# Optimization experiments

Hardware: AMD Instinct MI355X
Metric: run time of the kernel (lower is better)

Reference implementation:

```python
import jax, jax.numpy as jnp
import numpy as np
from jax import lax

K = 3; PAD = 1; STR = 1; DIL = 1; DG = 16; MRM = 10.0


def _conv3(x, w, b):
    y = lax.conv_general_dilated(x, w, (1, 1), ((PAD, PAD), (PAD, PAD)),
                                 dimension_numbers=('NCHW', 'OIHW', 'NCHW'))
    return y + b[None, :, None, None]


def _leaky(x):
    return jnp.where(x >= 0, x, 0.1 * x)


def _bilinear_gather(img, py, px):
    # img: [B, dg, cg, H, W]; py, px: [B, dg, KK, H, W] sampling coords
    B, dg, cg, H, W = img.shape
    KK = py.shape[2]
    y0f = jnp.floor(py); x0f = jnp.floor(px)
    wy = py - y0f; wx = px - x0f          # bilinear fractions (grad flows via py/px)
    y0 = y0f.astype(jnp.int32); x0 = x0f.astype(jnp.int32)
    y1 = y0 + 1; x1 = x0 + 1
    imgf = img.reshape(B * dg, cg, H * W)

    def gather(yi, xi):
        valid = ((yi >= 0) & (yi < H) & (xi >= 0) & (xi < W)).astype(img.dtype)
        idx = jnp.clip(yi, 0, H - 1) * W + jnp.clip(xi, 0, W - 1)
        idxf = idx.reshape(B * dg, KK * H * W)
        v = jax.vmap(lambda im, ix: im[:, ix])(imgf, idxf)  # [B*dg, cg, KK*H*W]
        v = v.reshape(B, dg, cg, KK, H, W)
        return v * valid[:, :, None]  # zero padding outside image

    w00 = ((1 - wy) * (1 - wx))[:, :, None]
    w01 = ((1 - wy) * wx)[:, :, None]
    w10 = (wy * (1 - wx))[:, :, None]
    w11 = (wy * wx)[:, :, None]
    return (gather(y0, x0) * w00 + gather(y0, x1) * w01 +
            gather(y1, x0) * w10 + gather(y1, x1) * w11)


def reference(x, extra_feat, flow, w1, b1, w2, b2, w3, b3, weight):
    B, C, H, W = x.shape
    KK = K * K
    cg = C // DG
    P = DG * KK
    # offset/mask generating convnet
    h = _leaky(_conv3(extra_feat, w1, b1))
    h = _leaky(_conv3(h, w2, b2))
    o = _conv3(h, w3, b3)                       # [B, 3*P, H, W]
    o1, o2, m = jnp.split(o, 3, axis=1)
    off = MRM * jnp.tanh(jnp.concatenate([o1, o2], axis=1))  # [B, 2P, H, W]
    flow_yx = flow[:, ::-1]                      # flip(1): (x,y)->(y,x)
    off = off + jnp.tile(flow_yx, (1, P, 1, 1))
    off = off.reshape(B, DG, KK, 2, H, W)        # pair p=(g,k): channel 2p=y, 2p+1=x
    off_y = off[:, :, :, 0]
    off_x = off[:, :, :, 1]
    mask = jax.nn.sigmoid(m).reshape(B, DG, KK, H, W)

    ki = jnp.arange(KK)
    ky = (ki // K).astype(x.dtype) * DIL - PAD   # kernel row offsets
    kx = (ki % K).astype(x.dtype) * DIL - PAD
    base_h = jnp.arange(H, dtype=x.dtype) * STR
    base_w = jnp.arange(W, dtype=x.dtype) * STR
    py = base_h[None, None, None, :, None] + ky[None, None, :, None, None] + off_y
    px = base_w[None, None, None, None, :] + kx[None, None, :, None, None] + off_x

    img = x.reshape(B, DG, cg, H, W)
    val = _bilinear_gather(img, py, px) * mask[:, :, None]  # [B,dg,cg,KK,H,W]
    wk = weight.reshape(weight.shape[0], DG, cg, KK)
    # modulated deformable conv accumulate (bias=None in original forward)
    return jnp.einsum('bgckhw,ogck->bohw', val, wk)


def setup_inputs() -> dict:
    key = jax.random.key(0)
    ks = jax.random.split(key, 10)
    B, C, H, W = 2, 64, 128, 128
    OFFC = 3 * K * K * DG  # 432
    return {
        'x': jax.random.normal(ks[0], (B, C, H, W), jnp.float32),
        'extra_feat': jax.random.normal(ks[1], (B, 2 * C, H, W), jnp.float32),
        'flow': jax.random.normal(ks[2], (B, 2, H, W), jnp.float32),
        'w1': jax.random.normal(ks[3], (C, 2 * C, 3, 3), jnp.float32) * 0.05,
        'b1': jnp.zeros((C,), jnp.float32),
        'w2': jax.random.normal(ks[4], (C, C, 3, 3), jnp.float32) * 0.05,
        'b2': jnp.zeros((C,), jnp.float32),
        'w3': jax.random.normal(ks[5], (OFFC, C, 3, 3), jnp.float32) * 0.01,
        'b3': jnp.zeros((OFFC,), jnp.float32),
        'weight': jax.random.normal(ks[6], (C, C, 3, 3), jnp.float32) * 0.05,
    }
```

## Files before the change

### kernel.cpp

```cpp
#include <hip/hip_runtime.h>
#include <math.h>

constexpr int B_   = 2;
constexpr int C_   = 64;
constexpr int H_   = 128;
constexpr int W_   = 128;
constexpr int HW_  = H_ * W_;
constexpr int DG_  = 16;
constexpr int KK_  = 9;
constexpr int CG_  = 4;
constexpr int OFFC_ = 3 * KK_ * DG_;
constexpr int R_   = C_ * KK_;
constexpr int WP_  = 130;
constexpr int HWP_ = WP_ * WP_;

typedef _Float16 half8 __attribute__((ext_vector_type(8)));
typedef _Float16 half4 __attribute__((ext_vector_type(4)));
typedef float floatx4 __attribute__((ext_vector_type(4)));

__device__ __forceinline__ void gl_lds16(const _Float16* g, _Float16* l)
{
    __builtin_amdgcn_global_load_lds(
        (const __attribute__((address_space(1))) void*)g,
        (__attribute__((address_space(3))) void*)l, 16, 0, 0);
}

__device__ __forceinline__ int afrag_src(int c)
{
    const int cmf = c >> 6, cq = (c >> 4) & 3, cl = c & 15;
    return (cmf * 16 + cl) * 32 + cq * 8;
}

template <int OC, int CIN>
__global__ __launch_bounds__(256) void prep_wA_k(
    const float* __restrict__ w, _Float16* __restrict__ wA)
{
    constexpr int CH = CIN / 32;
    const int j = blockIdx.x * 256 + threadIdx.x;
    if (j >= 9 * CH * OC * 32) return;
    const int slab = j / (OC * 32);
    const int rem  = j - slab * (OC * 32);
    const int oc   = rem >> 5;
    const int jj   = rem & 31;
    const int t    = slab / CH;
    const int h    = slab - t * CH;
    const int ic   = h * 32 + jj;
    wA[j] = (_Float16)w[(size_t)oc * (CIN * 9) + ic * 9 + t];
}

__global__ __launch_bounds__(256) void prep_wkA_k(
    const float* __restrict__ wk, _Float16* __restrict__ wkA)
{
    const int j = blockIdx.x * 256 + threadIdx.x;
    if (j >= 18 * 64 * 32) return;
    const int s   = j >> 11;
    const int rem = j & 2047;
    const int oc  = rem >> 5;
    const int jj  = rem & 31;
    const int k   = s >> 1;
    const int gc  = (s & 1) * 32 + jj;
    wkA[j] = (_Float16)wk[(size_t)oc * R_ + gc * 9 + k];
}

template <int CC>
__global__ __launch_bounds__(256) void nchw2slabpad_f16_k(
    const float* __restrict__ in, _Float16* __restrict__ outh)
{
    const int pix = blockIdx.x * 256 + threadIdx.x;
    const int b   = blockIdx.y;
    const int yp  = pix >> 7;
    const int xp  = pix & (W_ - 1);
    const float* ib = in + (size_t)b * CC * HW_ + pix;
#pragma unroll
    for (int c0 = 0; c0 < CC; c0 += 8) {
        half8 v;
#pragma unroll
        for (int j = 0; j < 8; ++j)
            v[j] = (_Float16)ib[(size_t)(c0 + j) * HW_];
        const int slab = c0 >> 5;
        *(half8*)&outh[((size_t)(slab * B_ + b) * HWP_
                        + (size_t)(yp + 1) * WP_ + (xp + 1)) * 32 + (c0 & 31)] = v;
    }
}

__global__ __launch_bounds__(256) void nchw2gx_f16_k(
    const float* __restrict__ in, _Float16* __restrict__ outh)
{
    const int pix = blockIdx.x * 256 + threadIdx.x;
    const int b   = blockIdx.y;
    const float* ib = in + (size_t)b * C_ * HW_ + pix;
#pragma unroll
    for (int g = 0; g < DG_; ++g) {
        half4 v;
#pragma unroll
        for (int c = 0; c < 4; ++c)
            v[c] = (_Float16)ib[(size_t)(g * 4 + c) * HW_];
        *(half4*)&outh[((size_t)(b * DG_ + g) * HW_ + pix) * 4] = v;
    }
}

__global__ __launch_bounds__(256, 2) void conv1_mfma_k(
    const _Float16* __restrict__ inp, const _Float16* __restrict__ wA,
    const float* __restrict__ bias, _Float16* __restrict__ outp)
{
    __shared__ __align__(16) _Float16 Asm[2 * 4096];

    const int tid  = threadIdx.x;
    const int lane = tid & 63;
    const int wv   = tid >> 6;
    const int l15  = lane & 15;
    const int quad = lane >> 4;

    const int zx   = blockIdx.x;
    const int row  = zx >> 1;
    const int b    = row >> 7;
    const int y    = row & 127;
    const int px0  = (zx & 1) * 64 + wv * 16;

    const int sA = afrag_src(tid);

    floatx4 acc[4];
#pragma unroll
    for (int mf = 0; mf < 4; ++mf)
        acc[mf] = (floatx4){0.f, 0.f, 0.f, 0.f};

    half8 Bf[2][2];

    gl_lds16(wA + 0 * 2048 + sA, Asm + 0 * 2048 + tid * 8);
    gl_lds16(wA + 1 * 2048 + sA, Asm + 1 * 2048 + tid * 8);
#pragma unroll
    for (int j = 0; j < 2; ++j)
        Bf[0][j] = *(const half8*)&inp[
            ((size_t)(j * B_ + b) * HWP_ + (size_t)(y + 0) * WP_
             + (px0 + l15 + 0)) * 32 + quad * 8];
    __syncthreads();

#pragma unroll
    for (int p = 0; p < 18; ++p) {
        const int cur = p & 1, nxt = cur ^ 1;
        if (p < 17) {
            const int ks0 = 2 * p + 2;
            const int t = ks0 >> 2;
            const int h0 = ks0 & 3;
            const int dy = t / 3, dx = t % 3;
#pragma unroll
            for (int j = 0; j < 2; ++j) {
                gl_lds16(wA + (size_t)(ks0 + j) * 2048 + sA,
                         Asm + (nxt * 2 + j) * 2048 + tid * 8);
                Bf[nxt][j] = *(const half8*)&inp[
                    ((size_t)((h0 + j) * B_ + b) * HWP_ + (size_t)(y + dy) * WP_
                     + (px0 + l15 + dx)) * 32 + quad * 8];
            }
        }
#pragma unroll
        for (int j = 0; j < 2; ++j) {
            const _Float16* abase = Asm + (cur * 2 + j) * 2048 + lane * 8;
#pragma unroll
            for (int mf = 0; mf < 4; ++mf) {
                const half8 afr = *(const half8*)&abase[mf * 512];
                acc[mf] = __builtin_amdgcn_mfma_f32_16x16x32_f16(afr, Bf[cur][j], acc[mf], 0, 0, 0);
            }
        }
        __syncthreads();
    }

#pragma unroll
    for (int mf = 0; mf < 4; ++mf) {
        const int oc4 = mf * 16 + quad * 4;
        const float4 b4 = *(const float4*)&bias[oc4];
        half4 v4;
#pragma unroll
        for (int reg = 0; reg < 4; ++reg) {
            float r = acc[mf][reg] + ((const float*)&b4)[reg];
            r = (r >= 0.f) ? r : 0.1f * r;
            v4[reg] = (_Float16)r;
        }
        *(half4*)&outp[((size_t)((oc4 >> 5) * B_ + b) * HWP_
                        + (size_t)(y + 1) * WP_ + (px0 + l15 + 1)) * 32 + (oc4 & 31)] = v4;
    }
}

__global__ __launch_bounds__(256, 2) void conv2_mfma_k(
    const _Float16* __restrict__ inp, const _Float16* __restrict__ wA,
    const float* __restrict__ bias, _Float16* __restrict__ outp)
{
    __shared__ __align__(16) _Float16 Asm[18 * 2048];

    const int tid  = threadIdx.x;
    const int lane = tid & 63;
    const int wv   = tid >> 6;
    const int l15  = lane & 15;
    const int quad = lane >> 4;

    const int zx   = blockIdx.x;
    const int row  = zx >> 1;
    const int b    = row >> 7;
    const int y    = row & 127;
    const int px0  = (zx & 1) * 64 + wv * 16;

    const int sA = afrag_src(tid);

#pragma unroll
    for (int s = 0; s < 18; ++s)
        gl_lds16(wA + (size_t)s * 2048 + sA, Asm + s * 2048 + tid * 8);

    const _Float16* bb[6];
#pragma unroll
    for (int h = 0; h < 2; ++h)
#pragma unroll
        for (int dy = 0; dy < 3; ++dy)
            bb[h * 3 + dy] = inp + ((size_t)(h * B_ + b) * HWP_
                                    + (size_t)(y + dy) * WP_ + px0 + l15) * 32 + quad * 8;

    floatx4 acc[4];
#pragma unroll
    for (int mf = 0; mf < 4; ++mf)
        acc[mf] = (floatx4){0.f, 0.f, 0.f, 0.f};

    __syncthreads();

    const _Float16* abase = Asm + lane * 8;
#pragma unroll
    for (int ks = 0; ks < 18; ++ks) {
        const int t = ks >> 1, h = ks & 1;
        const int dy = t / 3, dx = t % 3;
        const half8 bfr = *(const half8*)&bb[h * 3 + dy][dx * 32];
#pragma unroll
        for (int mf = 0; mf < 4; ++mf) {
            const half8 afr = *(const half8*)&abase[ks * 2048 + mf * 512];
            acc[mf] = __builtin_amdgcn_mfma_f32_16x16x32_f16(afr, bfr, acc[mf], 0, 0, 0);
        }
    }

#pragma unroll
    for (int mf = 0; mf < 4; ++mf) {
        const int oc4 = mf * 16 + quad * 4;
        const float4 b4 = *(const float4*)&bias[oc4];
        half4 v4;
#pragma unroll
        for (int reg = 0; reg < 4; ++reg) {
            float r = acc[mf][reg] + ((const float*)&b4)[reg];
            r = (r >= 0.f) ? r : 0.1f * r;
            v4[reg] = (_Float16)r;
        }
        *(half4*)&outp[((size_t)((oc4 >> 5) * B_ + b) * HWP_
                        + (size_t)(y + 1) * WP_ + (px0 + l15 + 1)) * 32 + (oc4 & 31)] = v4;
    }
}

__global__ __launch_bounds__(256, 3) void conv3_mfma_k(
    const _Float16* __restrict__ h2p, const _Float16* __restrict__ w3A,
    const float* __restrict__ bias, const float* __restrict__ flow,
    _Float16* __restrict__ omh)
{
    __shared__ __align__(16) _Float16 Smem[17 * 1536];
    _Float16* Lds = Smem;

    const int tid  = threadIdx.x;
    const int lane = tid & 63;
    const int wv   = tid >> 6;
    const int l15  = lane & 15;
    const int quad = lane >> 4;

    const int row = blockIdx.x;
    const int b   = row >> 7;
    const int y   = row & 127;
    const int m0  = blockIdx.y * 48;
    const int px0 = wv * 32;

#pragma unroll
    for (int r = 0; r < 13; ++r) {
        const int c = r * 256 + tid;
        if (c < 17 * 192) {
            const int ks = c / 192;
            const int cl = c - ks * 192;
            const int cmf = cl >> 6, cq = (cl >> 4) & 3, ccl = cl & 15;
            gl_lds16(w3A + ((size_t)ks * OFFC_ + m0 + cmf * 16 + ccl) * 32 + cq * 8,
                     Smem + c * 8);
        }
    }

    half8 Af17[3];
#pragma unroll
    for (int mf = 0; mf < 3; ++mf)
        Af17[mf] = *(const half8*)&w3A[
            ((size_t)17 * OFFC_ + m0 + mf * 16 + l15) * 32 + quad * 8];

    const _Float16* bb[6];
#pragma unroll
    for (int h = 0; h < 2; ++h)
#pragma unroll
        for (int dy = 0; dy < 3; ++dy)
            bb[h * 3 + dy] = h2p + ((size_t)(h * B_ + b) * HWP_
                                    + (size_t)(y + dy) * WP_ + px0 + l15) * 32 + quad * 8;

    floatx4 acc[3][2];
#pragma unroll
    for (int mf = 0; mf < 3; ++mf)
#pragma unroll
        for (int nf = 0; nf < 2; ++nf)
            acc[mf][nf] = (floatx4){0.f, 0.f, 0.f, 0.f};

    __syncthreads();

    const _Float16* abase = Smem + lane * 8;
#pragma unroll
    for (int ks = 0; ks < 17; ++ks) {
        const int t = ks >> 1, h = ks & 1;
        const int dy = t / 3, dx = t % 3;
        const half8 b0 = *(const half8*)&bb[h * 3 + dy][dx * 32];
        const half8 b1 = *(const half8*)&bb[h * 3 + dy][(16 + dx) * 32];
#pragma unroll
        for (int mf = 0; mf < 3; ++mf) {
            const half8 afr = *(const half8*)&abase[ks * 1536 + mf * 512];
            acc[mf][0] = __builtin_amdgcn_mfma_f32_16x16x32_f16(afr, b0, acc[mf][0], 0, 0, 0);
            acc[mf][1] = __builtin_amdgcn_mfma_f32_16x16x32_f16(afr, b1, acc[mf][1], 0, 0, 0);
        }
    }
    {
        const half8 b0 = *(const half8*)&bb[5][2 * 32];
        const half8 b1 = *(const half8*)&bb[5][(16 + 2) * 32];
#pragma unroll
        for (int mf = 0; mf < 3; ++mf) {
            acc[mf][0] = __builtin_amdgcn_mfma_f32_16x16x32_f16(Af17[mf], b0, acc[mf][0], 0, 0, 0);
            acc[mf][1] = __builtin_amdgcn_mfma_f32_16x16x32_f16(Af17[mf], b1, acc[mf][1], 0, 0, 0);
        }
    }
    __syncthreads();

    const bool is_off = (blockIdx.y < 6);
    float flY[2], flX[2];
#pragma unroll
    for (int nf = 0; nf < 2; ++nf) {
        const int px = px0 + nf * 16 + l15;
        if (is_off) {
            flY[nf] = flow[(size_t)(b * 2 + 1) * HW_ + y * W_ + px];
            flX[nf] = flow[(size_t)(b * 2 + 0) * HW_ + y * W_ + px];
        }
    }
#pragma unroll
    for (int mf = 0; mf < 3; ++mf) {
        const float4 b4 = *(const float4*)&bias[m0 + mf * 16 + quad * 4];
#pragma unroll
        for (int nf = 0; nf < 2; ++nf) {
            const int px = px0 + nf * 16 + l15;
#pragma unroll
            for (int reg = 0; reg < 4; ++reg) {
                const int ocl = mf * 16 + quad * 4 + reg;
                float val = acc[mf][nf][reg] + ((const float*)&b4)[reg];
                if (is_off) {
                    const int slot = reg & 1;
                    const float fl = slot ? flX[nf] : flY[nf];
                    const float e = __expf(2.f * val);
                    val = 10.f * (1.f - __fdividef(2.f, e + 1.f)) + fl;
                } else {
                    val = __fdividef(1.f, 1.f + __expf(-val));
                }
                Lds[ocl * 132 + px] = (_Float16)val;
            }
        }
    }
    __syncthreads();

#pragma unroll
    for (int it = 0; it < 6; ++it) {
        const int j4 = it * 256 + tid;
        const int r  = j4 >> 5;
        const int c4 = j4 & 31;
        const int oc = m0 + r;
        int g, k, slot;
        if (oc < 2 * DG_ * KK_) {
            g = oc / 18;
            const int rem = oc - g * 18;
            k = rem >> 1;
            slot = rem & 1;
        } else {
            const int c = oc - 2 * DG_ * KK_;
            g = c / 9;
            k = c - g * 9;
            slot = 2;
        }
        const half4 hv = *(const half4*)&Lds[r * 132 + c4 * 4];
        *(half4*)&omh[((size_t)((b * DG_ * KK_ + g * KK_ + k) * 3 + slot)) * HW_
                      + y * W_ + c4 * 4] = hv;
    }
}

__global__ __launch_bounds__(256) void gather_k(
    const _Float16* __restrict__ xg, const _Float16* __restrict__ omh,
    _Float16* __restrict__ valh)
{
    const int tid = threadIdx.x;
    const int pix = blockIdx.x * 256 + tid;
    const int zy  = blockIdx.y;
    const int b   = zy / KK_;
    const int k   = zy - b * KK_;
    const int yp  = pix >> 7;
    const int xp  = pix & (W_ - 1);
    const float fy = (float)(yp + (k / 3) - 1);
    const float fx = (float)(xp + (k % 3) - 1);

    half4 rec[16];
#pragma unroll
    for (int g = 0; g < DG_; ++g) {
        const size_t obase = ((size_t)((b * DG_ + g) * KK_ + k) * 3) * HW_ + pix;
        const float oy = (float)omh[obase];
        const float ox = (float)omh[obase + HW_];
        const float m  = (float)omh[obase + 2 * HW_];

        const float py = fy + oy;
        const float px = fx + ox;
        const float y0f = floorf(py);
        const float x0f = floorf(px);
        const float wy = py - y0f;
        const float wx = px - x0f;
        const int y0 = (int)y0f, x0 = (int)x0f;
        const int y1 = y0 + 1,  x1 = x0 + 1;
        const bool vy0 = ((unsigned)y0 < (unsigned)H_);
        const bool vy1 = ((unsigned)y1 < (unsigned)H_);
        const bool vx0 = ((unsigned)x0 < (unsigned)W_);
        const bool vx1 = ((unsigned)x1 < (unsigned)W_);
        const float w00 = vy0 && vx0 ? (1.f - wy) * (1.f - wx) : 0.f;
        const float w01 = vy0 && vx1 ? (1.f - wy) * wx         : 0.f;
        const float w10 = vy1 && vx0 ? wy * (1.f - wx)         : 0.f;
        const float w11 = vy1 && vx1 ? wy * wx                 : 0.f;
        const int i00 = (vy0 && vx0) ? y0 * W_ + x0 : 0;
        const int i01 = (vy0 && vx1) ? y0 * W_ + x1 : 0;
        const int i10 = (vy1 && vx0) ? y1 * W_ + x0 : 0;
        const int i11 = (vy1 && vx1) ? y1 * W_ + x1 : 0;

        const _Float16* xb = xg + (size_t)(b * DG_ + g) * HW_ * 4;
        const half4 p00 = *(const half4*)&xb[(size_t)i00 * 4];
        const half4 p01 = *(const half4*)&xb[(size_t)i01 * 4];
        const half4 p10 = *(const half4*)&xb[(size_t)i10 * 4];
        const half4 p11 = *(const half4*)&xb[(size_t)i11 * 4];

        half4 v4;
#pragma unroll
        for (int c = 0; c < CG_; ++c) {
            float v = w00 * (float)p00[c] + w01 * (float)p01[c]
                    + w10 * (float)p10[c] + w11 * (float)p11[c];
            v4[c] = (_Float16)(v * m);
        }
        rec[g] = v4;
    }

    _Float16* r0 = &valh[((size_t)((2 * k) * B_ + b) * HW_ + pix) * 32];
    _Float16* r1 = &valh[((size_t)((2 * k + 1) * B_ + b) * HW_ + pix) * 32];
#pragma unroll
    for (int j = 0; j < 4; ++j) {
        half8 w0, w1;
#pragma unroll
        for (int c = 0; c < 4; ++c) {
            w0[c]     = rec[2 * j][c];
            w0[c + 4] = rec[2 * j + 1][c];
            w1[c]     = rec[8 + 2 * j][c];
            w1[c + 4] = rec[9 + 2 * j][c];
        }
        *(half8*)&r0[j * 8] = w0;
        *(half8*)&r1[j * 8] = w1;
    }
}

__global__ __launch_bounds__(256, 2) void einsum_mfma_k(
    const _Float16* __restrict__ valh, const _Float16* __restrict__ wkA,
    float* __restrict__ out)
{
    __shared__ __align__(16) _Float16 Smem[18 * 2048];
    float* Lds = (float*)Smem;

    const int tid  = threadIdx.x;
    const int lane = tid & 63;
    const int wv   = tid >> 6;
    const int l15  = lane & 15;
    const int quad = lane >> 4;

    const int pixg0 = blockIdx.x * 64 + wv * 16;
    const int b     = pixg0 >> 14;
    const int pix0  = pixg0 & (HW_ - 1);

    const int sA = afrag_src(tid);

#pragma unroll
    for (int s = 0; s < 18; ++s)
        gl_lds16(wkA + (size_t)s * 2048 + sA, Smem + s * 2048 + tid * 8);

    floatx4 acc[4];
#pragma unroll
    for (int mf = 0; mf < 4; ++mf)
        acc[mf] = (floatx4){0.f, 0.f, 0.f, 0.f};

    half8 Bf[2];
    Bf[0] = *(const half8*)&valh[((size_t)(0 * B_ + b) * HW_ + pix0 + l15) * 32 + quad * 8];
    __syncthreads();

#pragma unroll
    for (int s = 0; s < 18; ++s) {
        const int cur = s & 1, nxt = cur ^ 1;
        if (s < 17) {
            const int s1 = s + 1;
            Bf[nxt] = *(const half8*)&valh[
                ((size_t)(s1 * B_ + b) * HW_ + pix0 + l15) * 32 + quad * 8];
        }
        const _Float16* abase = Smem + s * 2048 + lane * 8;
#pragma unroll
        for (int mf = 0; mf < 4; ++mf) {
            const half8 afr = *(const half8*)&abase[mf * 512];
            acc[mf] = __builtin_amdgcn_mfma_f32_16x16x32_f16(afr, Bf[cur], acc[mf], 0, 0, 0);
        }
    }
    __syncthreads();

    const int pxl = wv * 16 + l15;
#pragma unroll
    for (int mf = 0; mf < 4; ++mf)
#pragma unroll
        for (int reg = 0; reg < 4; ++reg)
            Lds[(mf * 16 + quad * 4 + reg) * 68 + pxl] = acc[mf][reg];
    __syncthreads();

    const int pixb = blockIdx.x * 64 & (HW_ - 1);
#pragma unroll
    for (int it = 0; it < 4; ++it) {
        const int j4 = it * 256 + tid;
        const int r  = j4 >> 4;
        const int c4 = j4 & 15;
        float4 v;
        v.x = Lds[r * 68 + c4 * 4 + 0];
        v.y = Lds[r * 68 + c4 * 4 + 1];
        v.z = Lds[r * 68 + c4 * 4 + 2];
        v.w = Lds[r * 68 + c4 * 4 + 3];
        *(float4*)&out[((size_t)(b * C_ + r)) * HW_ + pixb + c4 * 4] = v;
    }
}

extern "C" void kernel_launch(void* const* d_in, const int* in_sizes, int n_in,
                              void* d_out, int out_size, void* d_ws, size_t ws_size,
                              hipStream_t stream)
{
    const float* x    = (const float*)d_in[0];
    const float* ef   = (const float*)d_in[1];
    const float* flow = (const float*)d_in[2];
    const float* w1   = (const float*)d_in[3];
    const float* b1   = (const float*)d_in[4];
    const float* w2   = (const float*)d_in[5];
    const float* b2   = (const float*)d_in[6];
    const float* w3   = (const float*)d_in[7];
    const float* b3   = (const float*)d_in[8];
    const float* wk   = (const float*)d_in[9];
    float* out = (float*)d_out;

    _Float16* omh  = (_Float16*)d_ws;
    _Float16* valh = omh + (size_t)B_ * OFFC_ * HW_;
    _Float16* ef_p = valh + (size_t)18 * B_ * HW_ * 32;
    _Float16* xg   = ef_p + (size_t)4 * B_ * HWP_ * 32;
    _Float16* h1p  = xg + (size_t)B_ * HW_ * 64;
    _Float16* h2p  = h1p + (size_t)2 * B_ * HWP_ * 32;
    _Float16* w1A  = h2p + (size_t)2 * B_ * HWP_ * 32;
    _Float16* w2A  = w1A + 64 * 128 * 9;
    _Float16* w3A  = w2A + 64 * 64 * 9;
    _Float16* wkA  = w3A + OFFC_ * 64 * 9;

    hipMemsetAsync(ef_p, 0, (size_t)4 * B_ * HWP_ * 32 * 2, stream);
    hipMemsetAsync(h1p, 0, (size_t)2 * B_ * HWP_ * 32 * 2, stream);
    hipMemsetAsync(h2p, 0, (size_t)2 * B_ * HWP_ * 32 * 2, stream);

    prep_wA_k<64, 128><<<dim3((64 * 128 * 9 + 255) / 256), 256, 0, stream>>>(w1, w1A);
    prep_wA_k<64, 64><<<dim3((64 * 64 * 9 + 255) / 256), 256, 0, stream>>>(w2, w2A);
    prep_wA_k<OFFC_, 64><<<dim3((OFFC_ * 64 * 9 + 255) / 256), 256, 0, stream>>>(w3, w3A);
    prep_wkA_k<<<dim3((18 * 64 * 32 + 255) / 256), 256, 0, stream>>>(wk, wkA);
    nchw2slabpad_f16_k<128><<<dim3(HW_ / 256, B_), 256, 0, stream>>>(ef, ef_p);
    nchw2gx_f16_k<<<dim3(HW_ / 256, B_), 256, 0, stream>>>(x, xg);

    conv1_mfma_k<<<dim3(B_ * H_ * 2), 256, 0, stream>>>(ef_p, w1A, b1, h1p);
    conv2_mfma_k<<<dim3(B_ * H_ * 2), 256, 0, stream>>>(h1p, w2A, b2, h2p);
    conv3_mfma_k<<<dim3(B_ * H_, 9), 256, 0, stream>>>(h2p, w3A, b3, flow, omh);

    gather_k<<<dim3(HW_ / 256, B_ * KK_), 256, 0, stream>>>(xg, omh, valh);
    einsum_mfma_k<<<dim3(B_ * HW_ / 64), 256, 0, stream>>>(valh, wkA, out);
}
```

Measured before the change: 209.4 us.

## Stage conv1 weights in two bulk LDS phases and batch gather offset loads

In conv1_mfma_k, the per-step double-buffered weight staging with a barrier each step becomes two bulk phases: 18 weight slices (72 KB LDS) are loaded at once, then consumed with B fragments read from precomputed row pointers. This cuts the barrier count from 18 to a few. In gather_k, all 48 offset and mask loads are issued before any bilinear work so they are in flight together, and the kernel gets a launch-bounds occupancy hint. The large LDS allocation lowers the number of conv1 blocks that fit per CU, and the hoisted loads raise register pressure in gather_k.

```diff
diff --git a/kernel.cpp b/kernel.cpp
--- a/kernel.cpp
+++ b/kernel.cpp
@@ -103,7 +103,7 @@
     const _Float16* __restrict__ inp, const _Float16* __restrict__ wA,
     const float* __restrict__ bias, _Float16* __restrict__ outp)
 {
-    __shared__ __align__(16) _Float16 Asm[2 * 4096];
+    __shared__ __align__(16) _Float16 Asm[18 * 2048];
 
     const int tid  = threadIdx.x;
     const int lane = tid & 63;
@@ -119,49 +119,53 @@
 
     const int sA = afrag_src(tid);
 
+    const _Float16* bb[12];
+#pragma unroll
+    for (int h = 0; h < 4; ++h)
+#pragma unroll
+        for (int dy = 0; dy < 3; ++dy)
+            bb[h * 3 + dy] = inp + ((size_t)(h * B_ + b) * HWP_
+                                    + (size_t)(y + dy) * WP_ + px0 + l15) * 32 + quad * 8;
+
     floatx4 acc[4];
 #pragma unroll
     for (int mf = 0; mf < 4; ++mf)
         acc[mf] = (floatx4){0.f, 0.f, 0.f, 0.f};
 
-    half8 Bf[2][2];
-
-    gl_lds16(wA + 0 * 2048 + sA, Asm + 0 * 2048 + tid * 8);
-    gl_lds16(wA + 1 * 2048 + sA, Asm + 1 * 2048 + tid * 8);
-#pragma unroll
-    for (int j = 0; j < 2; ++j)
-        Bf[0][j] = *(const half8*)&inp[
-            ((size_t)(j * B_ + b) * HWP_ + (size_t)(y + 0) * WP_
-             + (px0 + l15 + 0)) * 32 + quad * 8];
-    __syncthreads();
-
-#pragma unroll
-    for (int p = 0; p < 18; ++p) {
-        const int cur = p & 1, nxt = cur ^ 1;
-        if (p < 17) {
-            const int ks0 = 2 * p + 2;
-            const int t = ks0 >> 2;
-            const int h0 = ks0 & 3;
-            const int dy = t / 3, dx = t % 3;
-#pragma unroll
-            for (int j = 0; j < 2; ++j) {
-                gl_lds16(wA + (size_t)(ks0 + j) * 2048 + sA,
-                         Asm + (nxt * 2 + j) * 2048 + tid * 8);
-                Bf[nxt][j] = *(const half8*)&inp[
-                    ((size_t)((h0 + j) * B_ + b) * HWP_ + (size_t)(y + dy) * WP_
-                     + (px0 + l15 + dx)) * 32 + quad * 8];
-            }
-        }
-#pragma unroll
-        for (int j = 0; j < 2; ++j) {
-            const _Float16* abase = Asm + (cur * 2 + j) * 2048 + lane * 8;
-#pragma unroll
-            for (int mf = 0; mf < 4; ++mf) {
-                const half8 afr = *(const half8*)&abase[mf * 512];
-                acc[mf] = __builtin_amdgcn_mfma_f32_16x16x32_f16(afr, Bf[cur][j], acc[mf], 0, 0, 0);
-            }
-        }
-        __syncthreads();
+#pragma unroll
+    for (int s = 0; s < 18; ++s)
+        gl_lds16(wA + (size_t)s * 2048 + sA, Asm + s * 2048 + tid * 8);
+    __syncthreads();
+
+    const _Float16* abase = Asm + lane * 8;
+#pragma unroll
+    for (int ks = 0; ks < 18; ++ks) {
+        const int t = ks >> 2, h = ks & 3;
+        const int dy = t / 3, dx = t % 3;
+        const half8 bfr = *(const half8*)&bb[h * 3 + dy][dx * 32];
+#pragma unroll
+        for (int mf = 0; mf < 4; ++mf) {
+            const half8 afr = *(const half8*)&abase[ks * 2048 + mf * 512];
+            acc[mf] = __builtin_amdgcn_mfma_f32_16x16x32_f16(afr, bfr, acc[mf], 0, 0, 0);
+        }
+    }
+    __syncthreads();
+
+#pragma unroll
+    for (int s = 0; s < 18; ++s)
+        gl_lds16(wA + (size_t)(18 + s) * 2048 + sA, Asm + s * 2048 + tid * 8);
+    __syncthreads();
+
+#pragma unroll
+    for (int ks = 18; ks < 36; ++ks) {
+        const int t = ks >> 2, h = ks & 3;
+        const int dy = t / 3, dx = t % 3;
+        const half8 bfr = *(const half8*)&bb[h * 3 + dy][dx * 32];
+#pragma unroll
+        for (int mf = 0; mf < 4; ++mf) {
+            const half8 afr = *(const half8*)&abase[(ks - 18) * 2048 + mf * 512];
+            acc[mf] = __builtin_amdgcn_mfma_f32_16x16x32_f16(afr, bfr, acc[mf], 0, 0, 0);
+        }
     }
 
 #pragma unroll
@@ -386,7 +390,7 @@
     }
 }
 
-__global__ __launch_bounds__(256) void gather_k(
+__global__ __launch_bounds__(256, 2) void gather_k(
     const _Float16* __restrict__ xg, const _Float16* __restrict__ omh,
     _Float16* __restrict__ valh)
 {
@@ -400,16 +404,20 @@
     const float fy = (float)(yp + (k / 3) - 1);
     const float fx = (float)(xp + (k % 3) - 1);
 
-    half4 rec[16];
+    float oyA[16], oxA[16], mA[16];
 #pragma unroll
     for (int g = 0; g < DG_; ++g) {
         const size_t obase = ((size_t)((b * DG_ + g) * KK_ + k) * 3) * HW_ + pix;
-        const float oy = (float)omh[obase];
-        const float ox = (float)omh[obase + HW_];
-        const float m  = (float)omh[obase + 2 * HW_];
-
-        const float py = fy + oy;
-        const float px = fx + ox;
+        oyA[g] = (float)omh[obase];
+        oxA[g] = (float)omh[obase + HW_];
+        mA[g]  = (float)omh[obase + 2 * HW_];
+    }
+
+    half4 rec[16];
+#pragma unroll
+    for (int g = 0; g < DG_; ++g) {
+        const float py = fy + oyA[g];
+        const float px = fx + oxA[g];
         const float y0f = floorf(py);
         const float x0f = floorf(px);
         const float wy = py - y0f;
@@ -440,7 +448,7 @@
         for (int c = 0; c < CG_; ++c) {
             float v = w00 * (float)p00[c] + w01 * (float)p01[c]
                     + w10 * (float)p10[c] + w11 * (float)p11[c];
-            v4[c] = (_Float16)(v * m);
+            v4[c] = (_Float16)(v * mA[g]);
         }
         rec[g] = v4;
     }
```

Result: no change. 206.3 us (-1.5%).
